# Kernel tuning notes

Measured on AMD Instinct MI355X. Metric: run time of the kernel, lower is better.

Reference implementation:

```python
import jax, jax.numpy as jnp
import numpy as np

NUM_NODES = 100000
NUM_EDGES = 1250000
NUM_GRAPHS = 1000
NUM_SHAPES = 8
NUM_COLORS = 8
NUM_REL = 3


def setup_inputs() -> dict:
    key = jax.random.key(0)
    ks = jax.random.split(key, 16)
    node_x = jax.random.randint(ks[0], (NUM_NODES, 2), 0, NUM_SHAPES)
    edge_index = jax.random.randint(ks[1], (2, NUM_EDGES), 0, NUM_NODES)
    edge_type = jax.random.randint(ks[2], (NUM_EDGES,), 0, NUM_REL)
    batch = jnp.sort(jax.random.randint(ks[3], (NUM_NODES,), 0, NUM_GRAPHS))
    sd = lambda fan_in: 1.0 / np.sqrt(fan_in)
    return {
        "node_x": node_x,
        "edge_index": edge_index,
        "edge_type": edge_type,
        "batch": batch,
        "pre_w": jax.random.normal(ks[4], (16, 32), jnp.float32) * sd(16),
        "pre_b": jnp.zeros((32,), jnp.float32),
        "conv1_w": jax.random.normal(ks[5], (NUM_REL, 32, 64), jnp.float32) * sd(32),
        "conv1_root": jax.random.normal(ks[6], (32, 64), jnp.float32) * sd(32),
        "conv1_b": jnp.zeros((64,), jnp.float32),
        "conv2_w": jax.random.normal(ks[7], (NUM_REL, 64, 64), jnp.float32) * sd(64),
        "conv2_root": jax.random.normal(ks[8], (64, 64), jnp.float32) * sd(64),
        "conv2_b": jnp.zeros((64,), jnp.float32),
        "cls_w": jax.random.normal(ks[9], (64, 10), jnp.float32) * sd(64),
        "cls_b": jnp.zeros((10,), jnp.float32),
    }


def rgcn_conv(x, edge_index, edge_type, W, root, b):
    # PyG RGCNConv: out = x @ root + b + sum_r mean_{j in N_r(i)} x_j @ W_r
    src, dst = edge_index[0], edge_index[1]
    n = x.shape[0]
    out = x @ root + b
    for r in range(NUM_REL):  # small fixed loop over relations
        mask = (edge_type == r).astype(x.dtype)           # [E]
        xr = x @ W[r]                                      # [N, d_out] dense GEMM once
        msg = xr[src] * mask[:, None]                      # gather + mask  [E, d_out]
        agg = jax.ops.segment_sum(msg, dst, num_segments=n)
        cnt = jax.ops.segment_sum(mask, dst, num_segments=n)
        out = out + agg / jnp.maximum(cnt, 1.0)[:, None]
    return out


def reference(node_x, edge_index, edge_type, batch, pre_w, pre_b,
              conv1_w, conv1_root, conv1_b, conv2_w, conv2_root, conv2_b,
              cls_w, cls_b):
    sx = jax.nn.one_hot(node_x[:, 0], NUM_SHAPES, dtype=pre_w.dtype)
    cx = jax.nn.one_hot(node_x[:, 1], NUM_COLORS, dtype=pre_w.dtype)
    x = jnp.concatenate([sx, cx], axis=1)                  # [N, 16]
    x = jax.nn.relu(x @ pre_w + pre_b)                     # [N, 32]
    x = jax.nn.relu(rgcn_conv(x, edge_index, edge_type, conv1_w, conv1_root, conv1_b))
    x = jax.nn.relu(rgcn_conv(x, edge_index, edge_type, conv2_w, conv2_root, conv2_b))
    # global mean pool over graphs
    gsum = jax.ops.segment_sum(x, batch, num_segments=NUM_GRAPHS)   # [G, 64]
    gcnt = jax.ops.segment_sum(jnp.ones((x.shape[0],), x.dtype), batch, num_segments=NUM_GRAPHS)
    pooled = gsum / jnp.maximum(gcnt, 1.0)[:, None]
    return pooled @ cls_w + cls_b                          # [G, 10]
```

## Files before the change

kernel.cpp:

```cpp
#include <hip/hip_runtime.h>

#define BSH 9
#define BNODES 512
#define NBLK_A 256

typedef __attribute__((ext_vector_type(8))) short short8;
typedef __attribute__((ext_vector_type(4))) float floatx4;

static __device__ inline float bf2f(unsigned short u) {
    union { unsigned int i; float f; } v; v.i = ((unsigned int)u) << 16; return v.f;
}
static __device__ inline unsigned f2bf(float f) {
    union { float f; unsigned int i; } v; v.f = f;
    unsigned int x = v.i;
    return (x + 0x7FFF + ((x >> 16) & 1)) >> 16;
}
static __device__ inline float asf(unsigned int u) {
    union { unsigned int i; float f; } v; v.i = u; return v.f;
}
static __device__ inline unsigned asu(float f) {
    union { float f; unsigned int i; } v; v.f = f; return v.i;
}

__global__ void __launch_bounds__(256) setup_kernel(
        const float* __restrict__ pre_w, const float* __restrict__ pre_b,
        const float* __restrict__ w1, const float* __restrict__ root1,
        const float* __restrict__ b1, const float* __restrict__ root2,
        const float* __restrict__ w2,
        unsigned short* __restrict__ B1f, float* __restrict__ root1t,
        unsigned short* __restrict__ B2f) {
    int combo = blockIdx.x;
    int t = threadIdx.x;
    __shared__ float x1s[32];
    if (t < 32) {
        int s = combo >> 3, c = combo & 7;
        float v = pre_w[s * 32 + t] + pre_w[(8 + c) * 32 + t] + pre_b[t];
        x1s[t] = v > 0.f ? v : 0.f;
    }
    __syncthreads();
    if (t < 64) {
        int j = t;
        float acc = b1[j];
#pragma unroll
        for (int k = 0; k < 32; ++k) acc = fmaf(x1s[k], root1[k * 64 + j], acc);
        root1t[combo * 64 + j] = acc;
        for (int r = 0; r < 3; ++r) {
            float a = 0.f;
#pragma unroll
            for (int k = 0; k < 32; ++k) a = fmaf(x1s[k], w1[(r * 32 + k) * 64 + j], a);
            int idx = (r << 6) | combo;
            int kt = idx >> 5, i = idx & 7, lrow = (idx >> 3) & 3;
            int nt = j >> 4;
            int l = (lrow << 4) | (j & 15);
            B1f[(((nt * 6 + kt) * 64) + l) * 8 + i] = (unsigned short)f2bf(a);
        }
    }
    {
        int tt = combo * 256 + t;
        int i = tt & 7, l = (tt >> 3) & 63, kt = (tt >> 9) & 1, nt = tt >> 10;
        int k = kt * 32 + ((l >> 4) * 8) + i;
        int col = nt * 16 + (l & 15);
        float v;
        if (col < 64) v = root2[k * 64 + col];
        else {
            int r = (col - 64) >> 6, wcol = (col - 64) & 63;
            v = w2[(r * 64 + k) * 64 + wcol];
        }
        B2f[tt] = (unsigned short)f2bf(v);
    }
}

__global__ void combo_kernel(const int* __restrict__ node_x, unsigned char* __restrict__ combo, int N) {
    int i = blockIdx.x * blockDim.x + threadIdx.x;
    if (i < N) combo[i] = (unsigned char)(node_x[2 * i] * 8 + node_x[2 * i + 1]);
}

__global__ void __launch_bounds__(256) hist_kernel(const int* __restrict__ ei,
                                                   int* __restrict__ hist, int E, int NB, int chunk) {
    __shared__ int lh[256];
    for (int t = threadIdx.x; t < NB; t += 256) lh[t] = 0;
    __syncthreads();
    int s = blockIdx.x * chunk, e1 = min(E, s + chunk);
    for (int e = s + threadIdx.x; e < e1; e += 256)
        atomicAdd(&lh[ei[E + e] >> BSH], 1);
    __syncthreads();
    for (int b = threadIdx.x; b < NB; b += 256) hist[b * NBLK_A + blockIdx.x] = lh[b];
}

__global__ void scan1(const int* __restrict__ in, int* __restrict__ out,
                      int* __restrict__ bsums, int n) {
    __shared__ int s[1024];
    int i = blockIdx.x * 1024 + threadIdx.x;
    int d = (i < n) ? in[i] : 0;
    s[threadIdx.x] = d;
    __syncthreads();
    for (int off = 1; off < 1024; off <<= 1) {
        int v = (threadIdx.x >= off) ? s[threadIdx.x - off] : 0;
        __syncthreads();
        s[threadIdx.x] += v;
        __syncthreads();
    }
    if (i < n) out[i] = s[threadIdx.x] - d;
    if (threadIdx.x == 1023) bsums[blockIdx.x] = s[1023];
}
__global__ void scan2(int* __restrict__ bsums, int nb) {
    __shared__ int s[128];
    int v = (threadIdx.x < nb) ? bsums[threadIdx.x] : 0;
    s[threadIdx.x] = v;
    __syncthreads();
    for (int off = 1; off < 128; off <<= 1) {
        int u = (threadIdx.x >= off) ? s[threadIdx.x - off] : 0;
        __syncthreads();
        s[threadIdx.x] += u;
        __syncthreads();
    }
    if (threadIdx.x < nb) bsums[threadIdx.x] = s[threadIdx.x] - v;
}
__global__ void scan3(int* __restrict__ out, const int* __restrict__ bsums, int n) {
    int i = blockIdx.x * 1024 + threadIdx.x;
    if (i < n) out[i] += bsums[blockIdx.x];
}

__global__ void __launch_bounds__(256) place_kernel(const int* __restrict__ ei, const int* __restrict__ et,
                                                    const int* __restrict__ off, unsigned* __restrict__ staged,
                                                    int E, int NB, int chunk) {
    __shared__ int lh[256];
    for (int t = threadIdx.x; t < NB; t += 256) lh[t] = 0;
    __syncthreads();
    int s = blockIdx.x * chunk, e1 = min(E, s + chunk);
    for (int e = s + threadIdx.x; e < e1; e += 256) {
        int d = ei[E + e];
        int b = d >> BSH;
        int lr = atomicAdd(&lh[b], 1);
        int pos = off[b * NBLK_A + blockIdx.x] + lr;
        staged[pos] = ((unsigned)(d & (BNODES - 1)) << 19) | ((unsigned)et[e] << 17) | (unsigned)ei[e];
    }
}

__global__ void __launch_bounds__(256) finalize_kernel(
        const unsigned* __restrict__ staged, const int* __restrict__ off,
        const unsigned char* __restrict__ combo,
        unsigned* __restrict__ edges1, uint2* __restrict__ edges2,
        int* __restrict__ base1, unsigned short* __restrict__ plen,
        int E, int N, int NB) {
    __shared__ int lrel[BNODES * 3];
    __shared__ float lwf[BNODES * 3];
    __shared__ int lcnt[BNODES];
    __shared__ int part[256];
    int blk = blockIdx.x;
    int d0 = blk * BNODES;
    int nn = min(BNODES, N - d0);
    int estart = off[blk * NBLK_A];
    int eend = (blk == NB - 1) ? E : off[(blk + 1) * NBLK_A];
    int ebase = estart + blk * (BNODES * 3);
    for (int t = threadIdx.x; t < BNODES * 3; t += 256) lrel[t] = 0;
    __syncthreads();
    for (int e = estart + threadIdx.x; e < eend; e += 256) {
        unsigned p = staged[e];
        atomicAdd(&lrel[(p >> 19) * 3 + ((p >> 17) & 3)], 1);
    }
    __syncthreads();
    for (int j = threadIdx.x; j < BNODES * 3; j += 256) {
        int c = lrel[j];
        lwf[j] = c ? 1.f / (float)c : 0.f;
    }
    int t = threadIdx.x;
    int n0 = 2 * t, n1 = 2 * t + 1;
    int ct0 = lrel[n0 * 3] + lrel[n0 * 3 + 1] + lrel[n0 * 3 + 2];
    int ct1 = lrel[n1 * 3] + lrel[n1 * 3 + 1] + lrel[n1 * 3 + 2];
    int pl0 = (ct0 + 3) & ~3, pl1 = (ct1 + 3) & ~3;
    int sum = pl0 + pl1;
    part[t] = sum;
    __syncthreads();
    for (int o = 1; o < 256; o <<= 1) {
        int u = (t >= o) ? part[t - o] : 0;
        __syncthreads();
        part[t] += u;
        __syncthreads();
    }
    int run = ebase + part[t] - sum;
    lcnt[n0] = run;
    lcnt[n1] = run + pl0;
    if (n0 < nn) { base1[d0 + n0] = run;       plen[d0 + n0] = (unsigned short)pl0; }
    if (n1 < nn) { base1[d0 + n1] = run + pl0; plen[d0 + n1] = (unsigned short)pl1; }
    if (blk == NB - 1 && t == 255) base1[N] = ebase + part[255];
    __syncthreads();
    for (int e = estart + threadIdx.x; e < eend; e += 256) {
        unsigned p = staged[e];
        int dloc = p >> 19;
        unsigned rel = (p >> 17) & 3;
        unsigned src = p & 0x1FFFF;
        float w = lwf[dloc * 3 + rel];
        int slot = atomicAdd(&lcnt[dloc], 1);
        uint2 e2;
        e2.x = (rel * (unsigned)N + src) * 16u;
        e2.y = asu(w);
        edges2[slot] = e2;
        edges1[slot] = (f2bf(w) << 16) | ((unsigned)(dloc & 63) << 8)
                     | (rel << 6) | (unsigned)combo[src];
    }
    __syncthreads();
    for (int n = threadIdx.x; n < nn; n += 256) {
        int ct = lrel[n * 3] + lrel[n * 3 + 1] + lrel[n * 3 + 2];
        int need = ((ct + 3) & ~3) - ct;
        int cur = lcnt[n];
        for (int k = 0; k < need; ++k) {
            uint2 z; z.x = 0u; z.y = 0u;
            edges2[cur + k] = z;
            edges1[cur + k] = 0u;
        }
    }
}

#define CSTR 196
__global__ void __launch_bounds__(512) conv1_mfma(
        const unsigned* __restrict__ edges1, const int* __restrict__ base1,
        const unsigned short* __restrict__ B1f, const float* __restrict__ root1t,
        const unsigned char* __restrict__ combo, unsigned short* __restrict__ h1, int N) {
    __shared__ float Cs[64 * CSTR];
    for (int t = threadIdx.x; t < 64 * CSTR; t += 512) Cs[t] = 0.f;
    __syncthreads();
    int g0 = blockIdx.x * 64;
    int gEnd = min(g0 + 64, N);
    int estart = base1[g0], eend = base1[gEnd];
    for (int e = estart + threadIdx.x; e < eend; e += 512) {
        unsigned ew = edges1[e];
        float wt = asf(ew & 0xFFFF0000u);
        int nl = (ew >> 8) & 63;
        int idx = ew & 255u;
        atomicAdd(&Cs[nl * CSTR + idx], wt);
    }
    __syncthreads();
    int lane = threadIdx.x & 63;
    int w0 = threadIdx.x >> 6;
    int tile = w0 >> 1;
    int node0 = g0 + 16 * tile;
    if (node0 >= N) return;
    int m = lane & 15, kg = lane >> 4;
    const float* cr = &Cs[(16 * tile + m) * CSTR];
    short8 a[6];
#pragma unroll
    for (int kt = 0; kt < 6; ++kt) {
        float4 ca = *(const float4*)(cr + kt * 32 + kg * 8);
        float4 cb = *(const float4*)(cr + kt * 32 + kg * 8 + 4);
        short8 av;
        av[0] = (short)f2bf(ca.x); av[1] = (short)f2bf(ca.y);
        av[2] = (short)f2bf(ca.z); av[3] = (short)f2bf(ca.w);
        av[4] = (short)f2bf(cb.x); av[5] = (short)f2bf(cb.y);
        av[6] = (short)f2bf(cb.z); av[7] = (short)f2bf(cb.w);
        a[kt] = av;
    }
#pragma unroll
    for (int nt2 = 0; nt2 < 2; ++nt2) {
        int nt = (w0 & 1) * 2 + nt2;
        floatx4 c = {0.f, 0.f, 0.f, 0.f};
#pragma unroll
        for (int kt = 0; kt < 6; ++kt) {
            short8 b = *(const short8*)(B1f + ((nt * 6 + kt) * 64 + lane) * 8);
            c = __builtin_amdgcn_mfma_f32_16x16x32_bf16(a[kt], b, c, 0, 0, 0);
        }
#pragma unroll
        for (int q = 0; q < 4; ++q) {
            int node = node0 + kg * 4 + q;
            if (node < N) {
                float v = c[q] + root1t[(int)combo[node] * 64 + nt * 16 + m];
                v = v > 0.f ? v : 0.f;
                h1[(size_t)node * 64 + nt * 16 + m] = (unsigned short)f2bf(v);
            }
        }
    }
}

__global__ void __launch_bounds__(256) gemm_Y(
        const unsigned short* __restrict__ h1, const unsigned short* __restrict__ B2f,
        const float* __restrict__ b2, unsigned short* __restrict__ Rb,
        unsigned short* __restrict__ Y, int N) {
    int g = blockIdx.x * 4 + (threadIdx.x >> 6);
    int node0 = g * 16;
    if (node0 >= N) return;
    int lane = threadIdx.x & 63;
    int m = lane & 15, kg = lane >> 4;
    short8 a[2];
#pragma unroll
    for (int kt = 0; kt < 2; ++kt)
        a[kt] = *(const short8*)(h1 + (size_t)(node0 + m) * 64 + kt * 32 + kg * 8);
#pragma unroll
    for (int nt = 0; nt < 16; ++nt) {
        floatx4 c = {0.f, 0.f, 0.f, 0.f};
#pragma unroll
        for (int kt = 0; kt < 2; ++kt) {
            short8 b = *(const short8*)(B2f + ((nt * 2 + kt) * 64 + lane) * 8);
            c = __builtin_amdgcn_mfma_f32_16x16x32_bf16(a[kt], b, c, 0, 0, 0);
        }
        if (nt < 4) {
            int col = nt * 16 + m;
            float bias = b2[col];
#pragma unroll
            for (int q = 0; q < 4; ++q) {
                int node = node0 + kg * 4 + q;
                if (node < N) Rb[(size_t)node * 64 + col] = (unsigned short)f2bf(c[q] + bias);
            }
        } else {
            int r = (nt - 4) >> 2;
            int ycol = ((nt - 4) & 3) * 16 + m;
#pragma unroll
            for (int q = 0; q < 4; ++q) {
                int node = node0 + kg * 4 + q;
                if (node < N)
                    Y[((size_t)r * N + node) * 64 + ycol] = (unsigned short)f2bf(c[q]);
            }
        }
    }
}

__global__ void __launch_bounds__(256) conv2_gather(
        const uint2* __restrict__ edges2, const int* __restrict__ base1,
        const unsigned short* __restrict__ plen, const uint4* __restrict__ Yu4,
        const uint4* __restrict__ Ru4, uint4* __restrict__ h2u4, int N) {
    int i = blockIdx.x * 8 + (threadIdx.x >> 5);
    if (i >= N) return;
    int l5 = threadIdx.x & 31;
    int el = l5 >> 3;
    int dl = l5 & 7;
    int s = base1[i];
    int L = plen[i];
    float f0 = 0.f, f1 = 0.f, f2 = 0.f, f3 = 0.f;
    float f4 = 0.f, f5 = 0.f, f6 = 0.f, f7 = 0.f;
    int t2 = 0;
    for (; t2 + 8 <= L; t2 += 8) {
        uint2 ea = edges2[s + t2 + el];
        uint2 eb = edges2[s + t2 + 4 + el];
        uint4 va = Yu4[(size_t)(ea.x >> 1) + dl];
        uint4 vb = Yu4[(size_t)(eb.x >> 1) + dl];
        float wa = asf(ea.y), wb = asf(eb.y);
        f0 = fmaf(wa, asf(va.x << 16), f0);
        f1 = fmaf(wa, asf(va.x & 0xFFFF0000u), f1);
        f2 = fmaf(wa, asf(va.y << 16), f2);
        f3 = fmaf(wa, asf(va.y & 0xFFFF0000u), f3);
        f4 = fmaf(wa, asf(va.z << 16), f4);
        f5 = fmaf(wa, asf(va.z & 0xFFFF0000u), f5);
        f6 = fmaf(wa, asf(va.w << 16), f6);
        f7 = fmaf(wa, asf(va.w & 0xFFFF0000u), f7);
        f0 = fmaf(wb, asf(vb.x << 16), f0);
        f1 = fmaf(wb, asf(vb.x & 0xFFFF0000u), f1);
        f2 = fmaf(wb, asf(vb.y << 16), f2);
        f3 = fmaf(wb, asf(vb.y & 0xFFFF0000u), f3);
        f4 = fmaf(wb, asf(vb.z << 16), f4);
        f5 = fmaf(wb, asf(vb.z & 0xFFFF0000u), f5);
        f6 = fmaf(wb, asf(vb.w << 16), f6);
        f7 = fmaf(wb, asf(vb.w & 0xFFFF0000u), f7);
    }
    if (t2 < L) {
        uint2 ea = edges2[s + t2 + el];
        uint4 va = Yu4[(size_t)(ea.x >> 1) + dl];
        float wa = asf(ea.y);
        f0 = fmaf(wa, asf(va.x << 16), f0);
        f1 = fmaf(wa, asf(va.x & 0xFFFF0000u), f1);
        f2 = fmaf(wa, asf(va.y << 16), f2);
        f3 = fmaf(wa, asf(va.y & 0xFFFF0000u), f3);
        f4 = fmaf(wa, asf(va.z << 16), f4);
        f5 = fmaf(wa, asf(va.z & 0xFFFF0000u), f5);
        f6 = fmaf(wa, asf(va.w << 16), f6);
        f7 = fmaf(wa, asf(va.w & 0xFFFF0000u), f7);
    }
    f0 += __shfl_xor(f0, 8); f0 += __shfl_xor(f0, 16);
    f1 += __shfl_xor(f1, 8); f1 += __shfl_xor(f1, 16);
    f2 += __shfl_xor(f2, 8); f2 += __shfl_xor(f2, 16);
    f3 += __shfl_xor(f3, 8); f3 += __shfl_xor(f3, 16);
    f4 += __shfl_xor(f4, 8); f4 += __shfl_xor(f4, 16);
    f5 += __shfl_xor(f5, 8); f5 += __shfl_xor(f5, 16);
    f6 += __shfl_xor(f6, 8); f6 += __shfl_xor(f6, 16);
    f7 += __shfl_xor(f7, 8); f7 += __shfl_xor(f7, 16);
    if (el == 0) {
        uint4 rb = Ru4[(size_t)i * 8 + dl];
        f0 += asf(rb.x << 16);
        f1 += asf(rb.x & 0xFFFF0000u);
        f2 += asf(rb.y << 16);
        f3 += asf(rb.y & 0xFFFF0000u);
        f4 += asf(rb.z << 16);
        f5 += asf(rb.z & 0xFFFF0000u);
        f6 += asf(rb.w << 16);
        f7 += asf(rb.w & 0xFFFF0000u);
        uint4 o;
        o.x = f2bf(f0) | (f2bf(f1) << 16);
        o.y = f2bf(f2) | (f2bf(f3) << 16);
        o.z = f2bf(f4) | (f2bf(f5) << 16);
        o.w = f2bf(f6) | (f2bf(f7) << 16);
        h2u4[(size_t)i * 8 + dl] = o;
    }
}

__global__ void __launch_bounds__(256) pool_cls(
        const unsigned short* __restrict__ h2, const int* __restrict__ batch,
        const float* __restrict__ cls_w, const float* __restrict__ cls_b,
        float* __restrict__ out, int N, int G) {
    int g = blockIdx.x;
    int lane = threadIdx.x & 63, w = threadIdx.x >> 6;
    auto lb = [&](int key) {
        int lo = 0, hi = N;
        while (lo < hi) { int mid = (lo + hi) >> 1; if (batch[mid] < key) lo = mid + 1; else hi = mid; }
        return lo;
    };
    int start = lb(g), end = lb(g + 1);
    float sum = 0.f;
    for (int i = start + w; i < end; i += 4) {
        float v = bf2f(h2[(size_t)i * 64 + lane]);
        sum += v > 0.f ? v : 0.f;
    }
    __shared__ float ps[4][64];
    ps[w][lane] = sum;
    __syncthreads();
    if (w == 0) {
        float tot = ps[0][lane] + ps[1][lane] + ps[2][lane] + ps[3][lane];
        int cntn = end - start;
        ps[0][lane] = tot / (float)(cntn > 0 ? cntn : 1);
    }
    __syncthreads();
    if (threadIdx.x < 10) {
        float o = cls_b[threadIdx.x];
#pragma unroll
        for (int j = 0; j < 64; ++j) o = fmaf(ps[0][j], cls_w[j * 10 + threadIdx.x], o);
        out[g * 10 + threadIdx.x] = o;
    }
}

extern "C" void kernel_launch(void* const* d_in, const int* in_sizes, int n_in,
                              void* d_out, int out_size, void* d_ws, size_t ws_size,
                              hipStream_t stream) {
    const int*   node_x = (const int*)d_in[0];
    const int*   ei     = (const int*)d_in[1];
    const int*   et     = (const int*)d_in[2];
    const int*   batch  = (const int*)d_in[3];
    const float* pre_w  = (const float*)d_in[4];
    const float* pre_b  = (const float*)d_in[5];
    const float* w1     = (const float*)d_in[6];
    const float* root1  = (const float*)d_in[7];
    const float* b1     = (const float*)d_in[8];
    const float* w2     = (const float*)d_in[9];
    const float* root2  = (const float*)d_in[10];
    const float* b2     = (const float*)d_in[11];
    const float* cls_w  = (const float*)d_in[12];
    const float* cls_b  = (const float*)d_in[13];
    float* out = (float*)d_out;

    int N = in_sizes[0] / 2;
    int E = in_sizes[1] / 2;
    int G = out_size / 10;

    int NB = (N + BNODES - 1) >> BSH;
    int chunk = (E + NBLK_A - 1) / NBLK_A;
    int nh = NB * NBLK_A;
    int nscan = (nh + 1023) / 1024;
    int EP = E + NB * BNODES * 3;

    char* ws = (char*)d_ws;
    size_t off_b = 0;
    auto alloc = [&](size_t bytes) {
        void* p = ws + off_b;
        off_b = (off_b + bytes + 255) & ~(size_t)255;
        return p;
    };
    unsigned short* B1f    = (unsigned short*)alloc(4 * 6 * 64 * 8 * sizeof(short));
    float*          root1t = (float*)alloc(64 * 64 * sizeof(float));
    unsigned short* B2f    = (unsigned short*)alloc(16 * 2 * 64 * 8 * sizeof(short));
    unsigned char*  combo  = (unsigned char*)alloc((size_t)N + 64);
    int*            hist   = (int*)alloc((size_t)nh * sizeof(int));
    int*            hoff   = (int*)alloc((size_t)nh * sizeof(int));
    int*            bsums  = (int*)alloc(128 * sizeof(int));
    unsigned*       staged = (unsigned*)alloc((size_t)E * sizeof(unsigned));
    unsigned*       edges1 = (unsigned*)alloc((size_t)EP * sizeof(unsigned));
    uint2*          edges2 = (uint2*)alloc(((size_t)EP + 16) * sizeof(uint2));
    int*            base1  = (int*)alloc(((size_t)N + 8) * sizeof(int));
    unsigned short* plen   = (unsigned short*)alloc(((size_t)N + 8) * sizeof(short));
    unsigned short* h1     = (unsigned short*)alloc((size_t)(N + 16) * 64 * sizeof(short));
    unsigned short* Rb     = (unsigned short*)alloc((size_t)N * 64 * sizeof(short));
    unsigned short* Y      = (unsigned short*)alloc((size_t)3 * N * 64 * sizeof(short));
    unsigned short* h2     = (unsigned short*)alloc((size_t)N * 64 * sizeof(short));

    setup_kernel<<<64, 256, 0, stream>>>(pre_w, pre_b, w1, root1, b1, root2, w2,
                                         B1f, root1t, B2f);
    combo_kernel<<<(N + 255) / 256, 256, 0, stream>>>(node_x, combo, N);

    hist_kernel<<<NBLK_A, 256, 0, stream>>>(ei, hist, E, NB, chunk);
    scan1<<<nscan, 1024, 0, stream>>>(hist, hoff, bsums, nh);
    scan2<<<1, 128, 0, stream>>>(bsums, nscan);
    scan3<<<nscan, 1024, 0, stream>>>(hoff, bsums, nh);
    place_kernel<<<NBLK_A, 256, 0, stream>>>(ei, et, hoff, staged, E, NB, chunk);
    finalize_kernel<<<NB, 256, 0, stream>>>(staged, hoff, combo, edges1, edges2,
                                            base1, plen, E, N, NB);

    conv1_mfma<<<(N + 63) / 64, 512, 0, stream>>>(edges1, base1, B1f, root1t, combo, h1, N);
    gemm_Y<<<((N + 15) / 16 + 3) / 4, 256, 0, stream>>>(h1, B2f, b2, Rb, Y, N);
    conv2_gather<<<(N + 7) / 8, 256, 0, stream>>>(edges2, base1, plen, (const uint4*)Y,
                                                  (const uint4*)Rb, (uint4*)h2, N);
    pool_cls<<<G, 256, 0, stream>>>(h2, batch, cls_w, cls_b, out, N, G);
}
```

Before: 169.4 us.

## Fuse conv1 MFMA with second-layer GEMM through shared memory

Merges the conv1 kernel and the gemm_Y kernel so each block keeps its 64-node h1 tile in LDS, reusing the Cs buffer, and immediately computes the root and relation projections for layer 2. This removes the global write and re-read of h1 and one kernel launch. In exchange it adds extra block-wide barriers and spreads the 16 output tiles across two waves per node tile. Out-of-range nodes now go through clamped combo reads instead of an early return.

```diff
diff --git a/kernel.cpp b/kernel.cpp
--- a/kernel.cpp
+++ b/kernel.cpp
@@ -213,11 +213,14 @@
 }
 
 #define CSTR 196
-__global__ void __launch_bounds__(512) conv1_mfma(
+__global__ void __launch_bounds__(512) conv1_fused(
         const unsigned* __restrict__ edges1, const int* __restrict__ base1,
         const unsigned short* __restrict__ B1f, const float* __restrict__ root1t,
-        const unsigned char* __restrict__ combo, unsigned short* __restrict__ h1, int N) {
+        const unsigned char* __restrict__ combo, const unsigned short* __restrict__ B2f,
+        const float* __restrict__ b2, unsigned short* __restrict__ Rb,
+        unsigned short* __restrict__ Y, int N) {
     __shared__ float Cs[64 * CSTR];
+    unsigned short* h1s = (unsigned short*)Cs;
     for (int t = threadIdx.x; t < 64 * CSTR; t += 512) Cs[t] = 0.f;
     __syncthreads();
     int g0 = blockIdx.x * 64;
@@ -226,16 +229,13 @@
     for (int e = estart + threadIdx.x; e < eend; e += 512) {
         unsigned ew = edges1[e];
         float wt = asf(ew & 0xFFFF0000u);
-        int nl = (ew >> 8) & 63;
-        int idx = ew & 255u;
-        atomicAdd(&Cs[nl * CSTR + idx], wt);
+        atomicAdd(&Cs[((ew >> 8) & 63) * CSTR + (ew & 255u)], wt);
     }
     __syncthreads();
     int lane = threadIdx.x & 63;
     int w0 = threadIdx.x >> 6;
     int tile = w0 >> 1;
     int node0 = g0 + 16 * tile;
-    if (node0 >= N) return;
     int m = lane & 15, kg = lane >> 4;
     const float* cr = &Cs[(16 * tile + m) * CSTR];
     short8 a[6];
@@ -250,6 +250,7 @@
         av[6] = (short)f2bf(cb.z); av[7] = (short)f2bf(cb.w);
         a[kt] = av;
     }
+    __syncthreads();
 #pragma unroll
     for (int nt2 = 0; nt2 < 2; ++nt2) {
         int nt = (w0 & 1) * 2 + nt2;
@@ -262,35 +263,25 @@
 #pragma unroll
         for (int q = 0; q < 4; ++q) {
             int node = node0 + kg * 4 + q;
-            if (node < N) {
-                float v = c[q] + root1t[(int)combo[node] * 64 + nt * 16 + m];
-                v = v > 0.f ? v : 0.f;
-                h1[(size_t)node * 64 + nt * 16 + m] = (unsigned short)f2bf(v);
-            }
-        }
-    }
-}
-
-__global__ void __launch_bounds__(256) gemm_Y(
-        const unsigned short* __restrict__ h1, const unsigned short* __restrict__ B2f,
-        const float* __restrict__ b2, unsigned short* __restrict__ Rb,
-        unsigned short* __restrict__ Y, int N) {
-    int g = blockIdx.x * 4 + (threadIdx.x >> 6);
-    int node0 = g * 16;
-    if (node0 >= N) return;
-    int lane = threadIdx.x & 63;
-    int m = lane & 15, kg = lane >> 4;
-    short8 a[2];
+            int cidx = combo[node < N ? node : N - 1];
+            float v = c[q] + root1t[cidx * 64 + nt * 16 + m];
+            v = v > 0.f ? v : 0.f;
+            h1s[(16 * tile + kg * 4 + q) * 68 + nt * 16 + m] = (unsigned short)f2bf(v);
+        }
+    }
+    __syncthreads();
+    short8 a2[2];
 #pragma unroll
     for (int kt = 0; kt < 2; ++kt)
-        a[kt] = *(const short8*)(h1 + (size_t)(node0 + m) * 64 + kt * 32 + kg * 8);
-#pragma unroll
-    for (int nt = 0; nt < 16; ++nt) {
+        a2[kt] = *(const short8*)&h1s[(16 * tile + m) * 68 + kt * 32 + kg * 8];
+#pragma unroll
+    for (int nt2 = 0; nt2 < 8; ++nt2) {
+        int nt = (w0 & 1) * 8 + nt2;
         floatx4 c = {0.f, 0.f, 0.f, 0.f};
 #pragma unroll
         for (int kt = 0; kt < 2; ++kt) {
             short8 b = *(const short8*)(B2f + ((nt * 2 + kt) * 64 + lane) * 8);
-            c = __builtin_amdgcn_mfma_f32_16x16x32_bf16(a[kt], b, c, 0, 0, 0);
+            c = __builtin_amdgcn_mfma_f32_16x16x32_bf16(a2[kt], b, c, 0, 0, 0);
         }
         if (nt < 4) {
             int col = nt * 16 + m;
@@ -472,7 +463,6 @@
     uint2*          edges2 = (uint2*)alloc(((size_t)EP + 16) * sizeof(uint2));
     int*            base1  = (int*)alloc(((size_t)N + 8) * sizeof(int));
     unsigned short* plen   = (unsigned short*)alloc(((size_t)N + 8) * sizeof(short));
-    unsigned short* h1     = (unsigned short*)alloc((size_t)(N + 16) * 64 * sizeof(short));
     unsigned short* Rb     = (unsigned short*)alloc((size_t)N * 64 * sizeof(short));
     unsigned short* Y      = (unsigned short*)alloc((size_t)3 * N * 64 * sizeof(short));
     unsigned short* h2     = (unsigned short*)alloc((size_t)N * 64 * sizeof(short));
@@ -489,8 +479,8 @@
     finalize_kernel<<<NB, 256, 0, stream>>>(staged, hoff, combo, edges1, edges2,
                                             base1, plen, E, N, NB);
 
-    conv1_mfma<<<(N + 63) / 64, 512, 0, stream>>>(edges1, base1, B1f, root1t, combo, h1, N);
-    gemm_Y<<<((N + 15) / 16 + 3) / 4, 256, 0, stream>>>(h1, B2f, b2, Rb, Y, N);
+    conv1_fused<<<(N + 63) / 64, 512, 0, stream>>>(edges1, base1, B1f, root1t, combo,
+                                                   B2f, b2, Rb, Y, N);
     conv2_gather<<<(N + 7) / 8, 256, 0, stream>>>(edges2, base1, plen, (const uint4*)Y,
                                                   (const uint4*)Rb, (uint4*)h2, N);
     pool_cls<<<G, 256, 0, stream>>>(h2, batch, cls_w, cls_b, out, N, G);
```

New measurement: 159.7 us. 1.06x faster.
